# Kernel tuning notes

Measured on AMD Instinct MI355X. Metric: run time of the kernel, lower is better.

## Reference

```python
import jax, jax.numpy as jnp
import numpy as np

B, N, K = 2, 2048, 32
NODE_IN, EDGE_IN, H, DEPTH = 64, 48, 128, 3
SCALE = 30.0
EPS = 1e-6


def _norm(x, g, b):
    # Ingraham-style Normalize: gain*(x-mu)/(std+eps)+bias, unbiased std
    mu = jnp.mean(x, axis=-1, keepdims=True)
    sigma = jnp.std(x, axis=-1, keepdims=True, ddof=1)
    return g * (x - mu) / (sigma + EPS) + b


def _gather_nodes(h, idx):
    # h: [B,N,C], idx: [B,N,K] -> [B,N,K,C]
    b, n, k = idx.shape
    flat = jnp.take_along_axis(h, idx.reshape(b, n * k, 1), axis=1)
    return flat.reshape(b, n, k, h.shape[-1])


def setup_inputs() -> dict:
    key = jax.random.key(0)
    ks = jax.random.split(key, 20)
    xav = lambda k, shp: jax.random.normal(k, shp, jnp.float32) * np.sqrt(2.0 / (shp[-2] + shp[-1]))
    return {
        "V": jax.random.normal(ks[0], (B, N, NODE_IN), jnp.float32),
        "E": jax.random.normal(ks[1], (B, N, K, EDGE_IN), jnp.float32),
        "hS": jax.random.normal(ks[2], (B, N, H), jnp.float32),
        "E_idx": jax.random.randint(ks[3], (B, N, K), 0, N, jnp.int32),
        "mask": jnp.ones((B, N), jnp.float32),
        "Wv_w": xav(ks[4], (NODE_IN, H)), "Wv_b": jnp.zeros((H,), jnp.float32),
        "Wv_g": jnp.ones((H,), jnp.float32), "Wv_b2": jnp.zeros((H,), jnp.float32),
        "We_w": xav(ks[5], (EDGE_IN, H)), "We_b": jnp.zeros((H,), jnp.float32),
        "We_g": jnp.ones((H,), jnp.float32), "We_b2": jnp.zeros((H,), jnp.float32),
        "Lw1": xav(ks[6], (DEPTH, 4 * H, H)), "Lb1": jnp.zeros((DEPTH, H), jnp.float32),
        "Lw2": xav(ks[7], (DEPTH, H, H)), "Lb2": jnp.zeros((DEPTH, H), jnp.float32),
        "Lw3": xav(ks[8], (DEPTH, H, H)), "Lb3": jnp.zeros((DEPTH, H), jnp.float32),
        "Ln_g": jnp.ones((DEPTH, H), jnp.float32), "Ln_b": jnp.zeros((DEPTH, H), jnp.float32),
    }


def reference(V, E, hS, E_idx, mask, Wv_w, Wv_b, Wv_g, Wv_b2, We_w, We_b, We_g, We_b2,
              Lw1, Lb1, Lw2, Lb2, Lw3, Lb3, Ln_g, Ln_b):
    h_v = _norm(V @ Wv_w + Wv_b, Wv_g, Wv_b2)          # [B,N,H]
    h_e = _norm(E @ We_w + We_b, We_g, We_b2)          # [B,N,K,H]
    nei_s = _gather_nodes(hS, E_idx)                   # [B,N,K,H]
    vmask = _gather_nodes(mask[..., None], E_idx)[..., 0]  # [B,N,K]
    h = h_v
    for i in range(DEPTH):
        nei_v = _gather_nodes(h, E_idx)                # [B,N,K,H]
        h_exp = jnp.broadcast_to(h[:, :, None, :], nei_v.shape)
        h_EV = jnp.concatenate([h_exp, nei_v, nei_s, h_e], axis=-1)  # [B,N,K,4H]
        m = jax.nn.relu(h_EV @ Lw1[i] + Lb1[i])
        m = jax.nn.relu(m @ Lw2[i] + Lb2[i])
        m = m @ Lw3[i] + Lb3[i]
        m = m * vmask[..., None]
        dh = jnp.sum(m, axis=-2) / SCALE               # [B,N,H]
        h = _norm(h + dh, Ln_g[i], Ln_b[i])            # dropout = identity (eval)
        h = h * mask[..., None]
    return h
```

## Files before the change

kernel.cpp:

```cpp
#include <hip/hip_runtime.h>
#include <hip/hip_bf16.h>

typedef unsigned short u16;
typedef unsigned int u32;
typedef __attribute__((ext_vector_type(8))) short short8;
typedef __attribute__((ext_vector_type(4))) float float4v;

#define DEV __device__ __forceinline__

constexpr int NN = 2048;
constexpr int BN = 4096;
constexpr int NEDGE = 131072;
constexpr float SCALE_INV = 1.0f / 30.0f;
constexpr float EPS = 1e-6f;

DEV u16 f2bf(float f) {
    u32 u = __float_as_uint(f);
    u32 r = (u + 0x7fffu + ((u >> 16) & 1u)) >> 16;
    return (u16)r;
}
DEV float bf2f(u16 v) { return __uint_as_float(((u32)v) << 16); }

__global__ __launch_bounds__(256, 3) void k_setup(
    const float* __restrict__ V, const float* __restrict__ E,
    const float* __restrict__ hS,
    const float* __restrict__ Vw_w, const float* __restrict__ Vw_b,
    const float* __restrict__ Vw_g, const float* __restrict__ Vw_b2,
    const float* __restrict__ We_w, const float* __restrict__ We_b,
    const float* __restrict__ We_g, const float* __restrict__ We_b2,
    const float* __restrict__ Lw1, const float* __restrict__ Lb1,
    const float* __restrict__ Lw2,
    float* __restrict__ hout, u16* __restrict__ he, u16* __restrict__ pack,
    float* __restrict__ P, float* __restrict__ G) {
    __shared__ __align__(16) char sBuf[34816];
    __shared__ float sSum[128 * 5];
    __shared__ float sSq[128 * 5];
    int b = blockIdx.x;
    int t = threadIdx.x;

    if (b < 1024) {
        float* sET = (float*)sBuf;
        u16* sOut = (u16*)sBuf;
        int L = t & 63, w = t >> 6;
        size_t rowbase = (size_t)b * 128;

        const float4v* src4 = (const float4v*)(E + rowbase * 48);
        #pragma unroll
        for (int i = 0; i < 6; i++) {
            int idx4 = t + i * 256;
            int r = idx4 / 12, c4 = (idx4 - r * 12) * 4;
            float4v v = src4[idx4];
            sET[(c4 + 0) * 130 + r] = v[0];
            sET[(c4 + 1) * 130 + r] = v[1];
            sET[(c4 + 2) * 130 + r] = v[2];
            sET[(c4 + 3) * 130 + r] = v[3];
        }
        __syncthreads();

        int wcol = __builtin_amdgcn_readfirstlane(w * 32);
        float4v acc0[8], acc1[8];
        #pragma unroll
        for (int ci = 0; ci < 8; ci++) {
            float4v bb = *(const float4v*)(We_b + wcol + ci * 4);
            acc0[ci] = bb;
            acc1[ci] = bb;
        }
        #pragma unroll 2
        for (int k = 0; k < 48; k++) {
            float2 e = *(const float2*)&sET[k * 130 + 2 * L];
            const float* wK = We_w + k * 128 + wcol;
            #pragma unroll
            for (int ci = 0; ci < 8; ci++) {
                float4v wv = *(const float4v*)(wK + ci * 4);
                acc0[ci] += e.x * wv;
                acc1[ci] += e.y * wv;
            }
        }

        float s0 = 0.f, q0 = 0.f, s1 = 0.f, q1 = 0.f;
        #pragma unroll
        for (int ci = 0; ci < 8; ci++) {
            #pragma unroll
            for (int p = 0; p < 4; p++) {
                float a0 = acc0[ci][p], a1 = acc1[ci][p];
                s0 += a0; q0 += a0 * a0;
                s1 += a1; q1 += a1 * a1;
            }
        }
        sSum[(2 * L) * 5 + w] = s0;     sSq[(2 * L) * 5 + w] = q0;
        sSum[(2 * L + 1) * 5 + w] = s1; sSq[(2 * L + 1) * 5 + w] = q1;
        __syncthreads();

        float fs0 = 0.f, fq0 = 0.f, fs1 = 0.f, fq1 = 0.f;
        #pragma unroll
        for (int j = 0; j < 4; j++) {
            fs0 += sSum[(2 * L) * 5 + j];     fq0 += sSq[(2 * L) * 5 + j];
            fs1 += sSum[(2 * L + 1) * 5 + j]; fq1 += sSq[(2 * L + 1) * 5 + j];
        }
        float mu0 = fs0 * (1.0f / 128.0f), mu1 = fs1 * (1.0f / 128.0f);
        float var0 = (fq0 - 128.0f * mu0 * mu0) * (1.0f / 127.0f);
        float var1 = (fq1 - 128.0f * mu1 * mu1) * (1.0f / 127.0f);
        float inv0 = 1.0f / (sqrtf(var0) + EPS);
        float inv1 = 1.0f / (sqrtf(var1) + EPS);

        u16* out0 = &sOut[(2 * L) * 136 + wcol];
        u16* out1 = &sOut[(2 * L + 1) * 136 + wcol];
        #pragma unroll
        for (int cc = 0; cc < 4; cc++) {
            u32 w0[4], w1[4];
            #pragma unroll
            for (int p = 0; p < 4; p++) {
                int c = cc * 8 + p * 2;
                int ci = c >> 2, pc = c & 3;
                float ga = We_g[wcol + c], gb = We_g[wcol + c + 1];
                float ba = We_b2[wcol + c], bb = We_b2[wcol + c + 1];
                float x0a = ga * (acc0[ci][pc] - mu0) * inv0 + ba;
                float x0b = gb * (acc0[ci][pc + 1] - mu0) * inv0 + bb;
                float x1a = ga * (acc1[ci][pc] - mu1) * inv1 + ba;
                float x1b = gb * (acc1[ci][pc + 1] - mu1) * inv1 + bb;
                w0[p] = (u32)f2bf(x0a) | ((u32)f2bf(x0b) << 16);
                w1[p] = (u32)f2bf(x1a) | ((u32)f2bf(x1b) << 16);
            }
            *(uint4*)(out0 + cc * 8) = make_uint4(w0[0], w0[1], w0[2], w0[3]);
            *(uint4*)(out1 + cc * 8) = make_uint4(w1[0], w1[1], w1[2], w1[3]);
        }
        __syncthreads();

        uint4* dst = (uint4*)(he + rowbase * 128);
        #pragma unroll
        for (int i = 0; i < 8; i++) {
            int c = t + i * 256;
            int row = c >> 4, m = c & 15;
            dst[c] = *(const uint4*)((const char*)sBuf + row * 272 + m * 16);
        }
    } else if (b < 1536) {
        float* sV = (float*)sBuf;
        float* sHn = ((float*)sBuf) + 512;
        float* sSn = ((float*)sBuf) + 1536;
        int nb = (b - 1024) * 8;
        #pragma unroll
        for (int i = 0; i < 2; i++) sV[t + i * 256] = V[(size_t)nb * 64 + t + i * 256];
        #pragma unroll
        for (int i = 0; i < 4; i++) sSn[t + i * 256] = hS[(size_t)nb * 128 + t + i * 256];
        __syncthreads();
        int g = t >> 5, L = t & 31;
        const float* v = &sV[g * 64];
        float a0 = Vw_b[L], a1 = Vw_b[L + 32], a2 = Vw_b[L + 64], a3 = Vw_b[L + 96];
        #pragma unroll 4
        for (int k = 0; k < 64; k++) {
            float vk = v[k];
            const float* wk = Vw_w + k * 128;
            a0 += vk * wk[L];
            a1 += vk * wk[L + 32];
            a2 += vk * wk[L + 64];
            a3 += vk * wk[L + 96];
        }
        float s = a0 + a1 + a2 + a3;
        float q = a0 * a0 + a1 * a1 + a2 * a2 + a3 * a3;
        #pragma unroll
        for (int o = 16; o > 0; o >>= 1) {
            s += __shfl_xor(s, o, 32);
            q += __shfl_xor(q, o, 32);
        }
        float mu = s * (1.0f / 128.0f);
        float var = (q - 128.0f * mu * mu) * (1.0f / 127.0f);
        float inv = 1.0f / (sqrtf(var) + EPS);
        float* outr = hout + (size_t)(nb + g) * 128;
        float o0 = Vw_g[L]      * (a0 - mu) * inv + Vw_b2[L];
        float o1 = Vw_g[L + 32] * (a1 - mu) * inv + Vw_b2[L + 32];
        float o2 = Vw_g[L + 64] * (a2 - mu) * inv + Vw_b2[L + 64];
        float o3 = Vw_g[L + 96] * (a3 - mu) * inv + Vw_b2[L + 96];
        outr[L] = o0; outr[L + 32] = o1; outr[L + 64] = o2; outr[L + 96] = o3;
        sHn[g * 128 + L] = o0;      sHn[g * 128 + L + 32] = o1;
        sHn[g * 128 + L + 64] = o2; sHn[g * 128 + L + 96] = o3;
        __syncthreads();
        int c = t & 127, pr = t >> 7;
        float p[4], gq[4];
        float b1 = Lb1[c];
        #pragma unroll
        for (int i = 0; i < 4; i++) { p[i] = b1; gq[i] = 0.f; }
        #pragma unroll 2
        for (int k = 0; k < 128; k++) {
            float wa = Lw1[k * 128 + c];
            float wb = Lw1[(128 + k) * 128 + c];
            float wc = Lw1[(256 + k) * 128 + c];
            #pragma unroll
            for (int i = 0; i < 4; i++) {
                float hk = sHn[(pr * 4 + i) * 128 + k];
                float sk = sSn[(pr * 4 + i) * 128 + k];
                p[i] += hk * wa;
                gq[i] += hk * wb + sk * wc;
            }
        }
        #pragma unroll
        for (int i = 0; i < 4; i++) {
            P[(size_t)(nb + pr * 4 + i) * 128 + c] = p[i];
            G[(size_t)(nb + pr * 4 + i) * 128 + c] = gq[i];
        }
    } else {
        int lm = b - 1536;
        const float* src;
        int slot = lm;
        if (lm < 6) {
            int l = lm >> 1, mat = lm & 1;
            src = (mat == 0) ? (Lw1 + ((size_t)l * 512 + 384) * 128)
                             : (Lw2 + (size_t)l * 16384);
        } else {
            int idx = lm - 6, ll = idx / 3, mi = idx - ll * 3;
            src = Lw1 + (((size_t)(ll + 1) * 512) + mi * 128) * 128;
        }
        u16* dst = pack + (size_t)slot * 16384;
        for (int i = 0; i < 64; i++) {
            int idx = t * 64 + i;
            int j = idx & 7, lane = (idx >> 3) & 63, s = (idx >> 9) & 3, tt = idx >> 11;
            int k = s * 32 + (lane >> 4) * 8 + j;
            int n = tt * 16 + (lane & 15);
            dst[idx] = f2bf(src[k * 128 + n]);
        }
    }
}

__global__ __launch_bounds__(256, 3) void k_edge_mlp(
    const u16* __restrict__ he, const float* __restrict__ Pcur,
    const float* __restrict__ Gcur, float* __restrict__ Pnext, float* __restrict__ Gnext,
    const int* __restrict__ Eidx, const float* __restrict__ maskp,
    const u16* __restrict__ pack, const float* __restrict__ Lb2,
    const float* __restrict__ Lw3, const float* __restrict__ Lb3,
    const float* __restrict__ Lng, const float* __restrict__ Lnb,
    const float* __restrict__ Lb1, const float* __restrict__ hS, int l,
    float* __restrict__ h, float* __restrict__ outp, int last) {
    __shared__ __align__(16) u16 sA[128 * 136];
    __shared__ __align__(16) u16 sHhi[4 * 136];
    __shared__ __align__(16) u16 sHlo[4 * 136];
    __shared__ __align__(16) u16 sShi[4 * 136];
    __shared__ __align__(16) u16 sSlo[4 * 136];
    __shared__ int sJ[128];
    __shared__ float sVm[128];
    __shared__ float sP[4 * 128];
    __shared__ float sM[4 * 128];
    __shared__ float sMs[4];
    __shared__ float sredS[4][2];
    __shared__ float sredQ[4][2];
    int nb = blockIdx.x * 4;
    int t = threadIdx.x;

    #pragma unroll
    for (int i = 0; i < 2; i++) {
        int idx = t + i * 256;
        int r = idx >> 7, c = idx & 127;
        float x = hS[(size_t)(nb + r) * 128 + c];
        u16 hb = f2bf(x);
        sShi[r * 136 + c] = hb;
        sSlo[r * 136 + c] = f2bf(x - bf2f(hb));
    }

    if (t < 128) {
        int gr = nb + (t >> 5);
        int j = Eidx[nb * 32 + t];
        int jg = (gr >> 11) * NN + j;
        sJ[t] = jg;
        sVm[t] = maskp[jg];
    }
    sP[t] = Pcur[(size_t)nb * 128 + t];
    sP[t + 256] = Pcur[(size_t)nb * 128 + 256 + t];
    {
        const uint4* src = (const uint4*)(he + (size_t)nb * 32 * 128);
        #pragma unroll
        for (int i = 0; i < 8; i++) {
            int idx = i * 256 + t;
            int row = idx >> 4, col = idx & 15;
            *(uint4*)(&sA[row * 136 + col * 8]) = src[idx];
        }
    }
    __syncthreads();

    if (t < 4) {
        float s = 0.f;
        #pragma unroll
        for (int e = 0; e < 32; e++) s += sVm[t * 32 + e];
        sMs[t] = s;
    }

    int w = t >> 6, lane = t & 63, q = lane >> 4, c16 = lane & 15;

    float gv[8][2][4];
    #pragma unroll
    for (int tm = 0; tm < 8; tm++)
        #pragma unroll
        for (int tn = 0; tn < 2; tn++) {
            int n = (2 * w + tn) * 16 + c16;
            #pragma unroll
            for (int r = 0; r < 4; r++) {
                int m = tm * 16 + q * 4 + r;
                gv[tm][tn][r] = Gcur[(size_t)sJ[m] * 128 + n];
            }
        }
    int cpost = t & 127, pr = t >> 7;
    int gr0 = nb + 2 * pr, gr1 = gr0 + 1;
    float h0 = h[(size_t)gr0 * 128 + cpost];
    float h1 = h[(size_t)gr1 * 128 + cpost];

    short8 Bf[2][4];
    const short8* pk1 = (const short8*)(pack + (size_t)(l * 2) * 16384);
    #pragma unroll
    for (int tn = 0; tn < 2; tn++)
        #pragma unroll
        for (int s = 0; s < 4; s++)
            Bf[tn][s] = pk1[((2 * w + tn) * 4 + s) * 64 + lane];

    float4v acc[8][2];
    #pragma unroll
    for (int tm = 0; tm < 8; tm++)
        #pragma unroll
        for (int tn = 0; tn < 2; tn++) acc[tm][tn] = (float4v){0.f, 0.f, 0.f, 0.f};

    #pragma unroll
    for (int tm = 0; tm < 8; tm++) {
        short8 a[4];
        #pragma unroll
        for (int s = 0; s < 4; s++)
            a[s] = *(const short8*)(&sA[(tm * 16 + c16) * 136 + s * 32 + q * 8]);
        #pragma unroll
        for (int s = 0; s < 4; s++) {
            acc[tm][0] = __builtin_amdgcn_mfma_f32_16x16x32_bf16(a[s], Bf[0][s], acc[tm][0], 0, 0, 0);
            acc[tm][1] = __builtin_amdgcn_mfma_f32_16x16x32_bf16(a[s], Bf[1][s], acc[tm][1], 0, 0, 0);
        }
    }
    __syncthreads();

    #pragma unroll
    for (int tm = 0; tm < 8; tm++) {
        #pragma unroll
        for (int tn = 0; tn < 2; tn++) {
            int n = (2 * w + tn) * 16 + c16;
            #pragma unroll
            for (int r = 0; r < 4; r++) {
                int m = tm * 16 + q * 4 + r;
                int g = m >> 5;
                float v = acc[tm][tn][r] + sP[g * 128 + n] + gv[tm][tn][r];
                v = v > 0.f ? v : 0.f;
                sA[m * 136 + n] = f2bf(v);
            }
        }
    }
    __syncthreads();

    const short8* pk2 = (const short8*)(pack + (size_t)(l * 2 + 1) * 16384);
    #pragma unroll
    for (int tn = 0; tn < 2; tn++)
        #pragma unroll
        for (int s = 0; s < 4; s++)
            Bf[tn][s] = pk2[((2 * w + tn) * 4 + s) * 64 + lane];
    #pragma unroll
    for (int tm = 0; tm < 8; tm++)
        #pragma unroll
        for (int tn = 0; tn < 2; tn++) acc[tm][tn] = (float4v){0.f, 0.f, 0.f, 0.f};
    #pragma unroll
    for (int tm = 0; tm < 8; tm++) {
        short8 a[4];
        #pragma unroll
        for (int s = 0; s < 4; s++)
            a[s] = *(const short8*)(&sA[(tm * 16 + c16) * 136 + s * 32 + q * 8]);
        #pragma unroll
        for (int s = 0; s < 4; s++) {
            acc[tm][0] = __builtin_amdgcn_mfma_f32_16x16x32_bf16(a[s], Bf[0][s], acc[tm][0], 0, 0, 0);
            acc[tm][1] = __builtin_amdgcn_mfma_f32_16x16x32_bf16(a[s], Bf[1][s], acc[tm][1], 0, 0, 0);
        }
    }

    float b2v0 = Lb2[l * 128 + (2 * w) * 16 + c16];
    float b2v1 = Lb2[l * 128 + (2 * w + 1) * 16 + c16];
    #pragma unroll
    for (int g = 0; g < 4; g++) {
        float p0 = 0.f, p1 = 0.f;
        #pragma unroll
        for (int half = 0; half < 2; half++) {
            int tm = 2 * g + half;
            #pragma unroll
            for (int r = 0; r < 4; r++) {
                int m = tm * 16 + q * 4 + r;
                float vm = sVm[m];
                float x0 = acc[tm][0][r] + b2v0; x0 = x0 > 0.f ? x0 : 0.f;
                float x1 = acc[tm][1][r] + b2v1; x1 = x1 > 0.f ? x1 : 0.f;
                p0 += vm * x0;
                p1 += vm * x1;
            }
        }
        p0 += __shfl_xor(p0, 16, 64); p0 += __shfl_xor(p0, 32, 64);
        p1 += __shfl_xor(p1, 16, 64); p1 += __shfl_xor(p1, 32, 64);
        if (lane < 32) {
            float val = (lane < 16) ? p0 : p1;
            int col = 32 * w + (lane & 31);
            sM[g * 128 + col] = val;
        }
    }
    __syncthreads();

    int c = cpost;
    int g0 = 2 * pr, g1 = g0 + 1;
    const float* W3 = Lw3 + (size_t)l * 16384;
    float d0 = 0.f, d1 = 0.f;
    #pragma unroll 4
    for (int k = 0; k < 128; k++) {
        float wk = W3[k * 128 + c];
        d0 += sM[g0 * 128 + k] * wk;
        d1 += sM[g1 * 128 + k] * wk;
    }
    float b3 = Lb3[l * 128 + c];
    float gg = Lng[l * 128 + c];
    float bn = Lnb[l * 128 + c];
    float x0 = h0 + (d0 + sMs[g0] * b3) * SCALE_INV;
    float x1 = h1 + (d1 + sMs[g1] * b3) * SCALE_INV;
    float s0 = x0, s1 = x1, q0 = x0 * x0, q1 = x1 * x1;
    #pragma unroll
    for (int o = 32; o > 0; o >>= 1) {
        s0 += __shfl_xor(s0, o, 64); q0 += __shfl_xor(q0, o, 64);
        s1 += __shfl_xor(s1, o, 64); q1 += __shfl_xor(q1, o, 64);
    }
    if (lane == 0) {
        sredS[w][0] = s0; sredS[w][1] = s1;
        sredQ[w][0] = q0; sredQ[w][1] = q1;
    }
    __syncthreads();
    int wb = 2 * pr;
    float S0 = sredS[wb][0] + sredS[wb + 1][0];
    float S1 = sredS[wb][1] + sredS[wb + 1][1];
    float Q0 = sredQ[wb][0] + sredQ[wb + 1][0];
    float Q1 = sredQ[wb][1] + sredQ[wb + 1][1];
    float mu0 = S0 * (1.0f / 128.0f), mu1 = S1 * (1.0f / 128.0f);
    float var0 = (Q0 - 128.0f * mu0 * mu0) * (1.0f / 127.0f);
    float var1 = (Q1 - 128.0f * mu1 * mu1) * (1.0f / 127.0f);
    float m0 = maskp[gr0], m1v = maskp[gr1];
    float o0 = (gg * (x0 - mu0) / (sqrtf(var0) + EPS) + bn) * m0;
    float o1 = (gg * (x1 - mu1) / (sqrtf(var1) + EPS) + bn) * m1v;
    h[(size_t)gr0 * 128 + c] = o0;
    h[(size_t)gr1 * 128 + c] = o1;
    if (last) {
        outp[(size_t)gr0 * 128 + c] = o0;
        outp[(size_t)gr1 * 128 + c] = o1;
        return;
    }

    {
        u16 hb0 = f2bf(o0);
        sHhi[g0 * 136 + c] = hb0;
        sHlo[g0 * 136 + c] = f2bf(o0 - bf2f(hb0));
        u16 hb1 = f2bf(o1);
        sHhi[g1 * 136 + c] = hb1;
        sHlo[g1 * 136 + c] = f2bf(o1 - bf2f(hb1));
    }
    __syncthreads();
    {
        const short8* pkA = (const short8*)(pack + (size_t)(6 + l * 3 + 0) * 16384);
        const short8* pkB = (const short8*)(pack + (size_t)(6 + l * 3 + 1) * 16384);
        const short8* pkC = (const short8*)(pack + (size_t)(6 + l * 3 + 2) * 16384);
        float4v accP[2], accG[2];
        #pragma unroll
        for (int tn = 0; tn < 2; tn++) {
            accP[tn] = (float4v){0.f, 0.f, 0.f, 0.f};
            accG[tn] = (float4v){0.f, 0.f, 0.f, 0.f};
        }
        short8 z8 = (short8){0, 0, 0, 0, 0, 0, 0, 0};
        #pragma unroll
        for (int s = 0; s < 4; s++) {
            short8 aHh = z8, aHl = z8, aSh = z8, aSl = z8;
            if (c16 < 4) {
                int off = c16 * 136 + s * 32 + q * 8;
                aHh = *(const short8*)&sHhi[off];
                aHl = *(const short8*)&sHlo[off];
                aSh = *(const short8*)&sShi[off];
                aSl = *(const short8*)&sSlo[off];
            }
            #pragma unroll
            for (int tn = 0; tn < 2; tn++) {
                int bi = ((2 * w + tn) * 4 + s) * 64 + lane;
                short8 bA = pkA[bi], bB = pkB[bi], bC = pkC[bi];
                accP[tn] = __builtin_amdgcn_mfma_f32_16x16x32_bf16(aHl, bA, accP[tn], 0, 0, 0);
                accP[tn] = __builtin_amdgcn_mfma_f32_16x16x32_bf16(aHh, bA, accP[tn], 0, 0, 0);
                accG[tn] = __builtin_amdgcn_mfma_f32_16x16x32_bf16(aHl, bB, accG[tn], 0, 0, 0);
                accG[tn] = __builtin_amdgcn_mfma_f32_16x16x32_bf16(aHh, bB, accG[tn], 0, 0, 0);
                accG[tn] = __builtin_amdgcn_mfma_f32_16x16x32_bf16(aSl, bC, accG[tn], 0, 0, 0);
                accG[tn] = __builtin_amdgcn_mfma_f32_16x16x32_bf16(aSh, bC, accG[tn], 0, 0, 0);
            }
        }
        if (lane < 16) {
            #pragma unroll
            for (int tn = 0; tn < 2; tn++) {
                int col = (2 * w + tn) * 16 + lane;
                float b1v = Lb1[(l + 1) * 128 + col];
                #pragma unroll
                for (int r = 0; r < 4; r++) {
                    Pnext[(size_t)(nb + r) * 128 + col] = accP[tn][r] + b1v;
                    Gnext[(size_t)(nb + r) * 128 + col] = accG[tn][r];
                }
            }
        }
    }
}

extern "C" void kernel_launch(void* const* d_in, const int* in_sizes, int n_in,
                              void* d_out, int out_size, void* d_ws, size_t ws_size,
                              hipStream_t stream) {
    const float* V     = (const float*)d_in[0];
    const float* E     = (const float*)d_in[1];
    const float* hS    = (const float*)d_in[2];
    const int*   Eidx  = (const int*)d_in[3];
    const float* maskp = (const float*)d_in[4];
    const float* Wv_w  = (const float*)d_in[5];
    const float* Wv_b  = (const float*)d_in[6];
    const float* Wv_g  = (const float*)d_in[7];
    const float* Wv_b2 = (const float*)d_in[8];
    const float* We_w  = (const float*)d_in[9];
    const float* We_b  = (const float*)d_in[10];
    const float* We_g  = (const float*)d_in[11];
    const float* We_b2 = (const float*)d_in[12];
    const float* Lw1   = (const float*)d_in[13];
    const float* Lb1   = (const float*)d_in[14];
    const float* Lw2   = (const float*)d_in[15];
    const float* Lb2   = (const float*)d_in[16];
    const float* Lw3   = (const float*)d_in[17];
    const float* Lb3   = (const float*)d_in[18];
    const float* Ln_g  = (const float*)d_in[19];
    const float* Ln_b  = (const float*)d_in[20];

    char* ws = (char*)d_ws;
    float* h    = (float*)ws; ws += (size_t)BN * 128 * 4;
    float* P0   = (float*)ws; ws += (size_t)BN * 128 * 4;
    float* G0   = (float*)ws; ws += (size_t)BN * 128 * 4;
    float* P1   = (float*)ws; ws += (size_t)BN * 128 * 4;
    float* G1   = (float*)ws; ws += (size_t)BN * 128 * 4;
    u16*   he   = (u16*)ws;   ws += (size_t)NEDGE * 128 * 2;
    u16*   pack = (u16*)ws;   ws += (size_t)12 * 16384 * 2;

    k_setup<<<1548, 256, 0, stream>>>(V, E, hS, Wv_w, Wv_b, Wv_g, Wv_b2,
                                      We_w, We_b, We_g, We_b2, Lw1, Lb1, Lw2,
                                      h, he, pack, P0, G0);
    for (int l = 0; l < 3; l++) {
        const float* Pc = (l & 1) ? P1 : P0;
        const float* Gc = (l & 1) ? G1 : G0;
        float* Pn = (l & 1) ? P0 : P1;
        float* Gn = (l & 1) ? G0 : G1;
        k_edge_mlp<<<BN / 4, 256, 0, stream>>>(he, Pc, Gc, Pn, Gn,
                                               Eidx, maskp, pack, Lb2,
                                               Lw3, Lb3, Ln_g, Ln_b, Lb1, hS, l,
                                               h, (float*)d_out, l == 2);
    }
}
```

Before: 270.2 us.

## Compute edge embedding GEMM with split-bf16 MFMA instead of scalar FMA

The edge-input projection in the setup kernel now runs on MFMA. E is split into bf16 high and low parts stored row-major in shared memory, and both parts are multiplied by bf16 weights with 16x16x32 MFMA instructions. Row statistics for the normalization are reduced with wave shuffles, and mean and inverse std are staged in shared memory before the normalized bf16 output is written. This removes the scalar FP32 FMA loop over the 48 inputs. In exchange, the weights are rounded to bf16, which adds some precision loss, and the output stores become scattered 16-bit writes.

```diff
diff --git a/kernel.cpp b/kernel.cpp
--- a/kernel.cpp
+++ b/kernel.cpp
@@ -32,97 +32,136 @@
     const float* __restrict__ Lw2,
     float* __restrict__ hout, u16* __restrict__ he, u16* __restrict__ pack,
     float* __restrict__ P, float* __restrict__ G) {
-    __shared__ __align__(16) char sBuf[34816];
-    __shared__ float sSum[128 * 5];
-    __shared__ float sSq[128 * 5];
+    __shared__ __align__(16) char sBuf[36864];
+    __shared__ float sSum[128 * 4];
+    __shared__ float sSq[128 * 4];
+    __shared__ float sMu[128];
+    __shared__ float sInv[128];
     int b = blockIdx.x;
     int t = threadIdx.x;
 
     if (b < 1024) {
-        float* sET = (float*)sBuf;
+        u16* sEh = (u16*)sBuf;
+        u16* sEl = (u16*)(sBuf + 18432);
         u16* sOut = (u16*)sBuf;
-        int L = t & 63, w = t >> 6;
+        int lane = t & 63, w = t >> 6, q = lane >> 4, c16 = lane & 15;
         size_t rowbase = (size_t)b * 128;
 
-        const float4v* src4 = (const float4v*)(E + rowbase * 48);
-        #pragma unroll
-        for (int i = 0; i < 6; i++) {
-            int idx4 = t + i * 256;
-            int r = idx4 / 12, c4 = (idx4 - r * 12) * 4;
-            float4v v = src4[idx4];
-            sET[(c4 + 0) * 130 + r] = v[0];
-            sET[(c4 + 1) * 130 + r] = v[1];
-            sET[(c4 + 2) * 130 + r] = v[2];
-            sET[(c4 + 3) * 130 + r] = v[3];
-        }
+        {
+            const float4v* src4 = (const float4v*)(E + rowbase * 48);
+            #pragma unroll
+            for (int i = 0; i < 6; i++) {
+                int idx4 = t + i * 256;
+                int r = idx4 / 12, c4 = (idx4 - r * 12) * 4;
+                float4v v = src4[idx4];
+                u32 hi0, hi1, lo0, lo1;
+                {
+                    u16 h0 = f2bf(v[0]), h1 = f2bf(v[1]);
+                    lo0 = (u32)f2bf(v[0] - bf2f(h0)) | ((u32)f2bf(v[1] - bf2f(h1)) << 16);
+                    hi0 = (u32)h0 | ((u32)h1 << 16);
+                    u16 h2 = f2bf(v[2]), h3 = f2bf(v[3]);
+                    lo1 = (u32)f2bf(v[2] - bf2f(h2)) | ((u32)f2bf(v[3] - bf2f(h3)) << 16);
+                    hi1 = (u32)h2 | ((u32)h3 << 16);
+                }
+                u32* dh = (u32*)(&sEh[r * 72 + c4]);
+                u32* dl = (u32*)(&sEl[r * 72 + c4]);
+                dh[0] = hi0; dh[1] = hi1;
+                dl[0] = lo0; dl[1] = lo1;
+            }
+            #pragma unroll
+            for (int i = 0; i < 4; i++) {
+                int idx = t + i * 256;
+                int r = idx >> 3, cc = idx & 7;
+                ((u32*)(&sEh[r * 72 + 48]))[cc] = 0;
+                ((u32*)(&sEl[r * 72 + 48]))[cc] = 0;
+            }
+        }
+
+        int n0 = (2 * w) * 16 + c16, n1 = n0 + 16;
+        short8 Bf[2][2];
+        #pragma unroll
+        for (int s = 0; s < 2; s++) {
+            #pragma unroll
+            for (int j = 0; j < 8; j++) {
+                int k = s * 32 + q * 8 + j;
+                float v0 = (k < 48) ? We_w[k * 128 + n0] : 0.f;
+                float v1 = (k < 48) ? We_w[k * 128 + n1] : 0.f;
+                Bf[0][s][j] = (short)f2bf(v0);
+                Bf[1][s][j] = (short)f2bf(v1);
+            }
+        }
+        float bias0 = We_b[n0], bias1 = We_b[n1];
+        float g0v = We_g[n0], g1v = We_g[n1];
+        float bb0 = We_b2[n0], bb1 = We_b2[n1];
         __syncthreads();
 
-        int wcol = __builtin_amdgcn_readfirstlane(w * 32);
-        float4v acc0[8], acc1[8];
-        #pragma unroll
-        for (int ci = 0; ci < 8; ci++) {
-            float4v bb = *(const float4v*)(We_b + wcol + ci * 4);
-            acc0[ci] = bb;
-            acc1[ci] = bb;
-        }
-        #pragma unroll 2
-        for (int k = 0; k < 48; k++) {
-            float2 e = *(const float2*)&sET[k * 130 + 2 * L];
-            const float* wK = We_w + k * 128 + wcol;
-            #pragma unroll
-            for (int ci = 0; ci < 8; ci++) {
-                float4v wv = *(const float4v*)(wK + ci * 4);
-                acc0[ci] += e.x * wv;
-                acc1[ci] += e.y * wv;
-            }
-        }
-
-        float s0 = 0.f, q0 = 0.f, s1 = 0.f, q1 = 0.f;
-        #pragma unroll
-        for (int ci = 0; ci < 8; ci++) {
-            #pragma unroll
-            for (int p = 0; p < 4; p++) {
-                float a0 = acc0[ci][p], a1 = acc1[ci][p];
-                s0 += a0; q0 += a0 * a0;
-                s1 += a1; q1 += a1 * a1;
-            }
-        }
-        sSum[(2 * L) * 5 + w] = s0;     sSq[(2 * L) * 5 + w] = q0;
-        sSum[(2 * L + 1) * 5 + w] = s1; sSq[(2 * L + 1) * 5 + w] = q1;
+        float4v acc[8][2];
+        #pragma unroll
+        for (int tm = 0; tm < 8; tm++) {
+            acc[tm][0] = (float4v){0.f, 0.f, 0.f, 0.f};
+            acc[tm][1] = (float4v){0.f, 0.f, 0.f, 0.f};
+        }
+        #pragma unroll
+        for (int tm = 0; tm < 8; tm++) {
+            int rowoff = (tm * 16 + c16) * 72 + q * 8;
+            short8 ah[2], al[2];
+            #pragma unroll
+            for (int s = 0; s < 2; s++) {
+                ah[s] = *(const short8*)(&sEh[rowoff + s * 32]);
+                al[s] = *(const short8*)(&sEl[rowoff + s * 32]);
+            }
+            #pragma unroll
+            for (int s = 0; s < 2; s++) {
+                acc[tm][0] = __builtin_amdgcn_mfma_f32_16x16x32_bf16(al[s], Bf[0][s], acc[tm][0], 0, 0, 0);
+                acc[tm][0] = __builtin_amdgcn_mfma_f32_16x16x32_bf16(ah[s], Bf[0][s], acc[tm][0], 0, 0, 0);
+                acc[tm][1] = __builtin_amdgcn_mfma_f32_16x16x32_bf16(al[s], Bf[1][s], acc[tm][1], 0, 0, 0);
+                acc[tm][1] = __builtin_amdgcn_mfma_f32_16x16x32_bf16(ah[s], Bf[1][s], acc[tm][1], 0, 0, 0);
+            }
+        }
+
+        #pragma unroll
+        for (int tm = 0; tm < 8; tm++) {
+            #pragma unroll
+            for (int r = 0; r < 4; r++) {
+                acc[tm][0][r] += bias0;
+                acc[tm][1][r] += bias1;
+                float v = acc[tm][0][r] + acc[tm][1][r];
+                float sq = acc[tm][0][r] * acc[tm][0][r] + acc[tm][1][r] * acc[tm][1][r];
+                #pragma unroll
+                for (int o = 1; o < 16; o <<= 1) {
+                    v += __shfl_xor(v, o, 64);
+                    sq += __shfl_xor(sq, o, 64);
+                }
+                if (c16 == 0) {
+                    int m = tm * 16 + q * 4 + r;
+                    sSum[m * 4 + w] = v;
+                    sSq[m * 4 + w] = sq;
+                }
+            }
+        }
         __syncthreads();
 
-        float fs0 = 0.f, fq0 = 0.f, fs1 = 0.f, fq1 = 0.f;
-        #pragma unroll
-        for (int j = 0; j < 4; j++) {
-            fs0 += sSum[(2 * L) * 5 + j];     fq0 += sSq[(2 * L) * 5 + j];
-            fs1 += sSum[(2 * L + 1) * 5 + j]; fq1 += sSq[(2 * L + 1) * 5 + j];
-        }
-        float mu0 = fs0 * (1.0f / 128.0f), mu1 = fs1 * (1.0f / 128.0f);
-        float var0 = (fq0 - 128.0f * mu0 * mu0) * (1.0f / 127.0f);
-        float var1 = (fq1 - 128.0f * mu1 * mu1) * (1.0f / 127.0f);
-        float inv0 = 1.0f / (sqrtf(var0) + EPS);
-        float inv1 = 1.0f / (sqrtf(var1) + EPS);
-
-        u16* out0 = &sOut[(2 * L) * 136 + wcol];
-        u16* out1 = &sOut[(2 * L + 1) * 136 + wcol];
-        #pragma unroll
-        for (int cc = 0; cc < 4; cc++) {
-            u32 w0[4], w1[4];
-            #pragma unroll
-            for (int p = 0; p < 4; p++) {
-                int c = cc * 8 + p * 2;
-                int ci = c >> 2, pc = c & 3;
-                float ga = We_g[wcol + c], gb = We_g[wcol + c + 1];
-                float ba = We_b2[wcol + c], bb = We_b2[wcol + c + 1];
-                float x0a = ga * (acc0[ci][pc] - mu0) * inv0 + ba;
-                float x0b = gb * (acc0[ci][pc + 1] - mu0) * inv0 + bb;
-                float x1a = ga * (acc1[ci][pc] - mu1) * inv1 + ba;
-                float x1b = gb * (acc1[ci][pc + 1] - mu1) * inv1 + bb;
-                w0[p] = (u32)f2bf(x0a) | ((u32)f2bf(x0b) << 16);
-                w1[p] = (u32)f2bf(x1a) | ((u32)f2bf(x1b) << 16);
-            }
-            *(uint4*)(out0 + cc * 8) = make_uint4(w0[0], w0[1], w0[2], w0[3]);
-            *(uint4*)(out1 + cc * 8) = make_uint4(w1[0], w1[1], w1[2], w1[3]);
+        if (t < 128) {
+            float4v sv = *(const float4v*)(&sSum[t * 4]);
+            float4v qv = *(const float4v*)(&sSq[t * 4]);
+            float S = sv[0] + sv[1] + sv[2] + sv[3];
+            float Q = qv[0] + qv[1] + qv[2] + qv[3];
+            float mu = S * (1.0f / 128.0f);
+            float var = (Q - 128.0f * mu * mu) * (1.0f / 127.0f);
+            sMu[t] = mu;
+            sInv[t] = 1.0f / (sqrtf(var) + EPS);
+        }
+        __syncthreads();
+
+        #pragma unroll
+        for (int tm = 0; tm < 8; tm++) {
+            #pragma unroll
+            for (int r = 0; r < 4; r++) {
+                int m = tm * 16 + q * 4 + r;
+                float mu = sMu[m], inv = sInv[m];
+                sOut[m * 136 + n0] = f2bf(g0v * (acc[tm][0][r] - mu) * inv + bb0);
+                sOut[m * 136 + n1] = f2bf(g1v * (acc[tm][1][r] - mu) * inv + bb1);
+            }
         }
         __syncthreads();
 
@@ -200,7 +239,6 @@
     } else {
         int lm = b - 1536;
         const float* src;
-        int slot = lm;
         if (lm < 6) {
             int l = lm >> 1, mat = lm & 1;
             src = (mat == 0) ? (Lw1 + ((size_t)l * 512 + 384) * 128)
@@ -209,7 +247,7 @@
             int idx = lm - 6, ll = idx / 3, mi = idx - ll * 3;
             src = Lw1 + (((size_t)(ll + 1) * 512) + mi * 128) * 128;
         }
-        u16* dst = pack + (size_t)slot * 16384;
+        u16* dst = pack + (size_t)lm * 16384;
         for (int i = 0; i < 64; i++) {
             int idx = t * 64 + i;
             int j = idx & 7, lane = (idx >> 3) & 63, s = (idx >> 9) & 3, tt = idx >> 11;
```

Measured after the change: 275.4 us. No clear change (+2.0%).
